# Performance work log

Hardware: AMD Instinct MI355X
Metric: run time of the kernel (lower is better)

## Reference

```python
import jax, jax.numpy as jnp
import numpy as np

# dims
N = 10000      # nodes
E = 320000     # edges (avg degree 32)
NS = 64        # hidden 0e scalar channels
NV = 64        # hidden 1o vector channels
EMB = 32       # node-attr embedding dim
NTYPES = 20    # max_atom_types
NB = 8         # number_of_basis (bessel)
RH = 16        # radial_neurons
L = 2          # layers
CUT = 3.5      # max_radius
NNEIGH = 32.0  # num_neighbors normalization
H = 0.1        # residual step size


def smooth_cutoff(u):
    # e3nn example smooth_cutoff applied to x/max_radius
    v = 2.0 * (u - 1.0)
    y = 0.5 * (1.0 - jnp.cos(jnp.pi * v))
    y = jnp.where(v > 0.0, 0.0, y)
    y = jnp.where(v < -1.0, 1.0, y)
    return y


def setup_inputs() -> dict:
    key = jax.random.key(0)
    ks = jax.random.split(key, 10)
    x = jax.random.normal(ks[0], (N, 6), jnp.float32)
    batch = jnp.zeros((N,), jnp.int32)
    node_attr = jax.random.randint(ks[1], (N,), 0, NTYPES)
    edge_src = jax.random.randint(ks[2], (E,), 0, N)
    # avoid self-loops (zero edge length -> NaN in sh / bessel)
    off = jax.random.randint(ks[3], (E,), 1, N)
    edge_dst = (edge_src + off) % N
    embed_table = 0.1 * jax.random.normal(ks[4], (NTYPES, EMB), jnp.float32)
    Ku = jax.random.normal(ks[5], (2, NV), jnp.float32)          # uplift (made semi-unitary via QR)
    W_sc_s = 0.05 * jax.random.normal(ks[6], (L, NS, EMB, NS + NV), jnp.float32)  # self-connection TP: scalars
    W_sc_v = 0.05 * jax.random.normal(ks[7], (L, NV, EMB, NV), jnp.float32)       # self-connection TP: vectors
    Wr1 = 0.3 * jax.random.normal(ks[8], (L, NB, RH), jnp.float32)
    br1 = jnp.zeros((L, RH), jnp.float32)
    Wr2 = 0.3 * jax.random.normal(ks[9], (L, RH, 4 * NV), jnp.float32)
    br2 = jnp.zeros((L, 4 * NV), jnp.float32)
    return {"x": x, "batch": batch, "node_attr": node_attr, "edge_src": edge_src,
            "edge_dst": edge_dst, "embed_table": embed_table, "Ku": Ku,
            "W_sc_s": W_sc_s, "W_sc_v": W_sc_v, "Wr1": Wr1, "br1": br1,
            "Wr2": Wr2, "br2": br2}


def reference(x, batch, node_attr, edge_src, edge_dst, embed_table, Ku,
              W_sc_s, W_sc_v, Wr1, br1, Wr2, br2):
    n = x.shape[0]
    a = embed_table[node_attr]                     # [n, EMB] node-attr embedding (0e scalars)
    # make uplift semi-unitary: Q^T Q = I_2
    Q, _ = jnp.linalg.qr(Ku.T)                     # [NV, 2]
    U = Q.T                                        # uplift [2, NV]
    x_v = x.reshape(n, 2, 3)                       # 2x1o: position, velocity
    y_s = jnp.zeros((n, NS), x.dtype)              # uplift has no 1o->0e path
    y_v = jnp.einsum('ncd,ch->nhd', x_v, U)        # [n, NV, 3]
    nfreq = jnp.arange(1, NB + 1, dtype=x.dtype)
    inv_deg = 1.0 / np.sqrt(NNEIGH)
    for l in range(L):
        pos = x_v[:, 0, :]
        ev = pos[edge_src] - pos[edge_dst]                          # [E, 3]
        elen = jnp.linalg.norm(ev, axis=1)                          # [E]
        sh = jnp.sqrt(3.0) * ev / elen[:, None]                     # 1x1o SH, component norm
        # bessel radial basis, scaled by sqrt(NB)
        bess = (jnp.sqrt(2.0 / CUT) * jnp.sin(jnp.pi * nfreq * elen[:, None] / CUT)
                / elen[:, None]) * np.sqrt(NB)                      # [E, NB]
        ea = smooth_cutoff(elen / CUT)[:, None] * sh                # edge_attr [E, 3]
        # radial MLP -> per-edge tensor-product weights (4 paths x NV channels)
        w = jax.nn.silu(bess @ Wr1[l] + br1[l]) @ Wr2[l] + br2[l]   # [E, 4*NV]
        wA, wB, wC, wD = jnp.split(w, 4, axis=1)
        s_src = y_s[edge_src]                                       # [E, NS]
        v_src = y_v[edge_src]                                       # [E, NV, 3]
        # TP paths: 0e x 1o -> 1o ; 1o x 1o -> 1o (cross) ; 1o x 1o -> 0e (dot, feats + gates)
        msg_v = (wA[:, :, None] * s_src[:, :, None] * ea[:, None, :]
                 + wC[:, :, None] * jnp.cross(v_src, ea[:, None, :]))  # [E, NV, 3]
        dots = jnp.einsum('evd,ed->ev', v_src, ea)                  # [E, NV]
        msg_s = jnp.concatenate([wB * dots, wD * dots], axis=1)     # [E, NS+NV]
        agg_s = jax.ops.segment_sum(msg_s, edge_dst, num_segments=n) * inv_deg
        agg_v = (jax.ops.segment_sum(msg_v.reshape(msg_v.shape[0], -1), edge_dst,
                                     num_segments=n).reshape(n, NV, 3) * inv_deg)
        # self-connection: fully-connected TP with node-attr scalars
        sc_s = jnp.einsum('ns,ne,seo->no', y_s, a, W_sc_s[l])       # [n, NS+NV]
        sc_v = jnp.einsum('nvd,ne,veu->nud', y_v, a, W_sc_v[l])     # [n, NV, 3]
        out_s = sc_s + agg_s
        out_v = sc_v + agg_v
        # gate: silu on scalar feats, sigmoid gates scale the vectors
        y_s = y_s + H * jax.nn.silu(out_s[:, :NS])
        y_v = y_v + H * jax.nn.sigmoid(out_s[:, NS:])[:, :, None] * out_v
        # project back to 2x1o
        x_v = jnp.einsum('nhd,hc->ncd', y_v, Q)
    return x_v.reshape(n, 6)
```

## Files before the change

### kernel.cpp

```cpp
#include <hip/hip_runtime.h>
#include <math.h>

#define NSC 64
#define NVC 64
#define EMB 32
#define NTYPES 20
#define NB 8
#define RH 16
#define LAYERS 2
#define CUTV 3.5f
#define HSTEP 0.1f

__global__ void qr_kernel(const float* __restrict__ Ku, float* __restrict__ Q)
{
  if (threadIdx.x != 0 || blockIdx.x != 0) return;
  float A0[64], A1[64], v0[64], v1[64], t1[64];
  for (int i = 0; i < 64; ++i) { A0[i] = Ku[i]; A1[i] = Ku[64 + i]; }
  float alpha = A0[0];
  float xn2 = 0.f;
  for (int i = 1; i < 64; ++i) xn2 += A0[i] * A0[i];
  float beta0 = -copysignf(sqrtf(alpha * alpha + xn2), alpha);
  float tau0 = (beta0 - alpha) / beta0;
  float inv0 = 1.f / (alpha - beta0);
  v0[0] = 1.f;
  for (int i = 1; i < 64; ++i) v0[i] = A0[i] * inv0;
  float w = 0.f;
  for (int i = 0; i < 64; ++i) w += v0[i] * A1[i];
  for (int i = 0; i < 64; ++i) A1[i] -= tau0 * w * v0[i];
  float alpha1 = A1[1];
  float xn2b = 0.f;
  for (int i = 2; i < 64; ++i) xn2b += A1[i] * A1[i];
  float beta1 = -copysignf(sqrtf(alpha1 * alpha1 + xn2b), alpha1);
  float tau1 = (beta1 - alpha1) / beta1;
  float inv1 = 1.f / (alpha1 - beta1);
  v1[0] = 0.f; v1[1] = 1.f;
  for (int i = 2; i < 64; ++i) v1[i] = A1[i] * inv1;
  for (int i = 0; i < 64; ++i) t1[i] = ((i == 1) ? 1.f : 0.f) - tau1 * v1[i];
  float d = 0.f;
  for (int i = 0; i < 64; ++i) d += v0[i] * t1[i];
  for (int i = 0; i < 64; ++i) {
    float q0 = ((i == 0) ? 1.f : 0.f) - tau0 * v0[i];
    float q1 = t1[i] - tau0 * d * v0[i];
    Q[i * 2 + 0] = q0;
    Q[i * 2 + 1] = q1;
  }
}

__global__ void init_state(const float* __restrict__ x, const float* __restrict__ Qm,
                           float* __restrict__ st0, int* __restrict__ cnt, int n)
{
  const int i = blockIdx.x * 256 + threadIdx.x;
  const int node = i >> 6, lane = i & 63;
  if (node < n) {
    const float q0 = Qm[lane * 2 + 0], q1 = Qm[lane * 2 + 1];
    const float* xp = x + (size_t)node * 6;
    float* sp = st0 + (size_t)node * 256 + lane;
    sp[0]   = 0.f;
    sp[64]  = xp[0] * q0 + xp[3] * q1;
    sp[128] = xp[1] * q0 + xp[4] * q1;
    sp[192] = xp[2] * q0 + xp[5] * q1;
  }
  if (i < n) cnt[i] = 0;
}

__global__ void hist_kernel(const int* __restrict__ edst, int* __restrict__ cnt, int m)
{
  const int e = blockIdx.x * 256 + threadIdx.x;
  if (e < m) atomicAdd(&cnt[edst[e]], 1);
}

__global__ void scan_kernel(int* cnt, int* off, int n)
{
  __shared__ int lds[1024];
  const int t = threadIdx.x;
  const int CH = (n + 1023) >> 10;
  const int base = t * CH;
  int local[16];
  int run = 0;
  for (int j = 0; j < CH; ++j) {
    int v = (base + j < n) ? cnt[base + j] : 0;
    local[j] = run;
    run += v;
  }
  lds[t] = run;
  __syncthreads();
  for (int s = 1; s < 1024; s <<= 1) {
    int v = (t >= s) ? lds[t - s] : 0;
    __syncthreads();
    lds[t] += v;
    __syncthreads();
  }
  const int excl = lds[t] - run;
  for (int j = 0; j < CH; ++j) {
    if (base + j < n) {
      int o = excl + local[j];
      off[base + j] = o;
      cnt[base + j] = o;
    }
  }
  if (t == 1023) off[n] = lds[1023];
}

__global__ void scatter_kernel(const int* __restrict__ edst, int* __restrict__ cursor,
                               int* __restrict__ csr, int m)
{
  const int e = blockIdx.x * 256 + threadIdx.x;
  if (e < m) {
    int p = atomicAdd(&cursor[edst[e]], 1);
    csr[p] = e;
  }
}

__global__ void reorder_kernel(const int* __restrict__ csr,
                               const int* __restrict__ esrc, const int* __restrict__ edst,
                               int* __restrict__ esrc_s, int* __restrict__ edst_s, int m)
{
  const int k = blockIdx.x * 256 + threadIdx.x;
  if (k < m) {
    const int e = csr[k];
    esrc_s[k] = esrc[e];
    edst_s[k] = edst[e];
  }
}

__global__ void type_weights(const float* __restrict__ embed,
                             const float* __restrict__ Wss,
                             const float* __restrict__ Wsv,
                             float* __restrict__ Ws, float* __restrict__ Wv,
                             int total_s, int total_v)
{
  const int i = blockIdx.x * 256 + threadIdx.x;
  if (i < total_s) {
    const int bid = i >> 13;
    const int p = i & 8191;
    const int l = bid / NTYPES, t = bid % NTYPES;
    const int s = p >> 7, o = p & 127;
    const float* ar = embed + t * EMB;
    const float* wp = Wss + ((size_t)(l * 64 + s) * EMB) * 128 + o;
    float acc = 0.f;
    #pragma unroll
    for (int e = 0; e < EMB; ++e) acc = fmaf(ar[e], wp[e * 128], acc);
    Ws[i] = acc;
  } else {
    const int j = i - total_s;
    if (j < total_v) {
      const int bid = j >> 12;
      const int p = j & 4095;
      const int l = bid / NTYPES, t = bid % NTYPES;
      const int v = p >> 6, u = p & 63;
      const float* ar = embed + t * EMB;
      const float* wp = Wsv + ((size_t)(l * 64 + v) * EMB) * 64 + u;
      float acc = 0.f;
      #pragma unroll
      for (int e = 0; e < EMB; ++e) acc = fmaf(ar[e], wp[e * 64], acc);
      Wv[j] = acc;
    }
  }
}

__global__ void edge_geom(const float* __restrict__ xv,
                          const int* __restrict__ esrc_s, const int* __restrict__ edst_s,
                          const float* __restrict__ Wr1l, const float* __restrict__ br1l,
                          float* __restrict__ egeo, int m)
{
  const int k = blockIdx.x * 256 + threadIdx.x;
  if (k >= m) return;
  const int s = esrc_s[k], d = edst_s[k];
  const float ex = xv[(size_t)s * 6 + 0] - xv[(size_t)d * 6 + 0];
  const float ey = xv[(size_t)s * 6 + 1] - xv[(size_t)d * 6 + 1];
  const float ez = xv[(size_t)s * 6 + 2] - xv[(size_t)d * 6 + 2];
  const float len = sqrtf(ex * ex + ey * ey + ez * ez);
  const float invl = 1.f / len;
  const float u = len * (1.f / CUTV);
  const float vv = 2.f * (u - 1.f);
  float cut = 0.5f * (1.f - cosf((float)M_PI * vv));
  cut = (vv > 0.f) ? 0.f : cut;
  cut = (vv < -1.f) ? 1.f : cut;
  const float cc = cut * 1.7320508075688772f * invl;
  float4* outp = (float4*)(egeo + (size_t)k * 20);
  outp[0] = make_float4(cc * ex, cc * ey, cc * ez, 0.f);
  float bess[NB];
  const float amp = 2.1380899352993948f * invl;
  const float arg = (float)M_PI * len * (1.f / CUTV);
  #pragma unroll
  for (int kk = 0; kk < NB; ++kk) bess[kk] = amp * sinf(arg * (float)(kk + 1));
  float hid[RH];
  #pragma unroll
  for (int j = 0; j < RH; ++j) {
    float h = br1l[j];
    #pragma unroll
    for (int kk = 0; kk < NB; ++kk) h = fmaf(bess[kk], Wr1l[kk * RH + j], h);
    hid[j] = h / (1.f + expf(-h));
  }
  outp[1] = make_float4(hid[0], hid[1], hid[2], hid[3]);
  outp[2] = make_float4(hid[4], hid[5], hid[6], hid[7]);
  outp[3] = make_float4(hid[8], hid[9], hid[10], hid[11]);
  outp[4] = make_float4(hid[12], hid[13], hid[14], hid[15]);
}

#define MLP_STEP(h, idx)                                                     \
  wA = fmaf((h), wr2A[idx], wA);                                             \
  wB = fmaf((h), wr2B[idx], wB);                                             \
  wC = fmaf((h), wr2C[idx], wC);                                             \
  wD = fmaf((h), wr2D[idx], wD);

__global__ __launch_bounds__(256, 2) void gather_update(
    const int* __restrict__ off, const int* __restrict__ esrc_s,
    const float* __restrict__ egeo,
    const float* __restrict__ st_in, const int* __restrict__ nattr,
    const float* __restrict__ Ws, const float* __restrict__ Wv,
    const float* __restrict__ Wr2l, const float* __restrict__ br2l,
    const float* __restrict__ Qm,
    float* __restrict__ st_out, float* __restrict__ xv_out, int n)
{
  const int lane = threadIdx.x & 63;
  const int node = blockIdx.x * 4 + (threadIdx.x >> 6);
  if (node >= n) return;

  float wr2A[RH], wr2B[RH], wr2C[RH], wr2D[RH];
  #pragma unroll
  for (int j = 0; j < RH; ++j) {
    const float* r = Wr2l + j * 256 + lane;
    wr2A[j] = r[0]; wr2B[j] = r[64]; wr2C[j] = r[128]; wr2D[j] = r[192];
  }
  const float bA = br2l[lane], bB = br2l[64 + lane],
              bC = br2l[128 + lane], bD = br2l[192 + lane];

  float aS1 = 0.f, aS2 = 0.f, aV0 = 0.f, aV1 = 0.f, aV2 = 0.f;
  const int k0 = off[node], k1 = off[node + 1];
  if (k0 < k1) {
    int srcN = esrc_s[k0];
    const float4* gN = (const float4*)(egeo + (size_t)k0 * 20);
    float4 N0 = gN[0], N1 = gN[1], N2 = gN[2], N3 = gN[3], N4 = gN[4];
    for (int k = k0; k < k1; ++k) {
      const int srcC = srcN;
      const float4 C0 = N0, C1 = N1, C2 = N2, C3 = N3, C4 = N4;
      const int kn = (k + 1 < k1) ? (k + 1) : k;
      srcN = esrc_s[kn];
      const float4* gp = (const float4*)(egeo + (size_t)kn * 20);
      N0 = gp[0]; N1 = gp[1]; N2 = gp[2]; N3 = gp[3]; N4 = gp[4];
      const float* pC = st_in + (size_t)srcC * 256 + lane;
      const float ss = pC[0], vx = pC[64], vy = pC[128], vz = pC[192];
      float wA = bA, wB = bB, wC = bC, wD = bD;
      MLP_STEP(C1.x, 0)  MLP_STEP(C1.y, 1)  MLP_STEP(C1.z, 2)  MLP_STEP(C1.w, 3)
      MLP_STEP(C2.x, 4)  MLP_STEP(C2.y, 5)  MLP_STEP(C2.z, 6)  MLP_STEP(C2.w, 7)
      MLP_STEP(C3.x, 8)  MLP_STEP(C3.y, 9)  MLP_STEP(C3.z, 10) MLP_STEP(C3.w, 11)
      MLP_STEP(C4.x, 12) MLP_STEP(C4.y, 13) MLP_STEP(C4.z, 14) MLP_STEP(C4.w, 15)
      const float dt = vx * C0.x + vy * C0.y + vz * C0.z;
      aS1 = fmaf(wB, dt, aS1);
      aS2 = fmaf(wD, dt, aS2);
      const float t = wA * ss;
      aV0 += t * C0.x + wC * (vy * C0.z - vz * C0.y);
      aV1 += t * C0.y + wC * (vz * C0.x - vx * C0.z);
      aV2 += t * C0.z + wC * (vx * C0.y - vy * C0.x);
    }
  }
  const float inv_deg = 0.17677669529663687f;

  const int ty = nattr[node];
  const float* WsT = Ws + (size_t)ty * 8192;
  const float* WvT = Wv + (size_t)ty * 4096;
  const float* own = st_in + (size_t)node * 256 + lane;
  const float ys_own = own[0], v0x = own[64], v0y = own[128], v0z = own[192];
  float oS1 = 0.f, oS2 = 0.f, oV0 = 0.f, oV1 = 0.f, oV2 = 0.f;
  #pragma unroll 4
  for (int s2 = 0; s2 < 64; ++s2) {
    const float yss = __shfl(ys_own, s2, 64);
    const float b0 = __shfl(v0x, s2, 64);
    const float b1 = __shfl(v0y, s2, 64);
    const float b2 = __shfl(v0z, s2, 64);
    const float wsA = WsT[s2 * 128 + lane];
    const float wsB = WsT[s2 * 128 + 64 + lane];
    const float wvv = WvT[s2 * 64 + lane];
    oS1 = fmaf(yss, wsA, oS1);
    oS2 = fmaf(yss, wsB, oS2);
    oV0 = fmaf(b0, wvv, oV0);
    oV1 = fmaf(b1, wvv, oV1);
    oV2 = fmaf(b2, wvv, oV2);
  }
  const float outS1 = oS1 + aS1 * inv_deg;
  const float outS2 = oS2 + aS2 * inv_deg;
  const float sig1 = 1.f / (1.f + expf(-outS1));
  const float gate = 1.f / (1.f + expf(-outS2));
  const float ysn = ys_own + HSTEP * outS1 * sig1;
  const float gf = HSTEP * gate;
  const float yvn0 = v0x + gf * (oV0 + aV0 * inv_deg);
  const float yvn1 = v0y + gf * (oV1 + aV1 * inv_deg);
  const float yvn2 = v0z + gf * (oV2 + aV2 * inv_deg);
  float* op = st_out + (size_t)node * 256 + lane;
  op[0] = ysn; op[64] = yvn0; op[128] = yvn1; op[192] = yvn2;

  const float q0 = Qm[lane * 2 + 0], q1 = Qm[lane * 2 + 1];
  float pr[6] = { yvn0 * q0, yvn1 * q0, yvn2 * q0,
                  yvn0 * q1, yvn1 * q1, yvn2 * q1 };
  #pragma unroll
  for (int mm = 1; mm < 64; mm <<= 1) {
    #pragma unroll
    for (int i = 0; i < 6; ++i) pr[i] += __shfl_xor(pr[i], mm, 64);
  }
  if (lane == 0) {
    #pragma unroll
    for (int i = 0; i < 6; ++i) xv_out[(size_t)node * 6 + i] = pr[i];
  }
}

extern "C" void kernel_launch(void* const* d_in, const int* in_sizes, int n_in,
                              void* d_out, int out_size, void* d_ws, size_t ws_size,
                              hipStream_t stream)
{
  const float* x     = (const float*)d_in[0];
  const int*   nattr = (const int*)d_in[2];
  const int*   esrc  = (const int*)d_in[3];
  const int*   edst  = (const int*)d_in[4];
  const float* embed = (const float*)d_in[5];
  const float* Ku    = (const float*)d_in[6];
  const float* Wss   = (const float*)d_in[7];
  const float* Wsv   = (const float*)d_in[8];
  const float* Wr1   = (const float*)d_in[9];
  const float* br1   = (const float*)d_in[10];
  const float* Wr2   = (const float*)d_in[11];
  const float* br2   = (const float*)d_in[12];
  const int n = in_sizes[0] / 6;
  const int m = in_sizes[3];

  char* p = (char*)d_ws;
  auto alloc = [&](size_t bytes) -> char* {
    char* r = p;
    p += (bytes + 255) & ~(size_t)255;
    return r;
  };
  int*   off    = (int*)alloc((size_t)(n + 1) * 4);
  int*   cursor = (int*)alloc((size_t)n * 4);
  int*   csr    = (int*)alloc((size_t)m * 4);
  int*   esrc_s = (int*)alloc((size_t)m * 4);
  int*   edst_s = (int*)alloc((size_t)m * 4);
  float* Q      = (float*)alloc(128 * 4);
  float* Ws     = (float*)alloc((size_t)LAYERS * NTYPES * 64 * 128 * 4);
  float* Wv     = (float*)alloc((size_t)LAYERS * NTYPES * 64 * 64 * 4);
  float* st0    = (float*)alloc((size_t)n * 256 * 4);
  float* st1    = (float*)alloc((size_t)n * 256 * 4);
  float* xvb    = (float*)alloc((size_t)n * 6 * 4);
  float* egeo   = (float*)alloc((size_t)m * 20 * 4);

  const int total_s = LAYERS * NTYPES * 64 * 128;
  const int total_v = LAYERS * NTYPES * 64 * 64;

  qr_kernel<<<1, 64, 0, stream>>>(Ku, Q);
  init_state<<<(n * 64 + 255) / 256, 256, 0, stream>>>(x, Q, st0, cursor, n);
  hist_kernel<<<(m + 255) / 256, 256, 0, stream>>>(edst, cursor, m);
  scan_kernel<<<1, 1024, 0, stream>>>(cursor, off, n);
  scatter_kernel<<<(m + 255) / 256, 256, 0, stream>>>(edst, cursor, csr, m);
  reorder_kernel<<<(m + 255) / 256, 256, 0, stream>>>(csr, esrc, edst, esrc_s, edst_s, m);
  type_weights<<<(total_s + total_v + 255) / 256, 256, 0, stream>>>(
      embed, Wss, Wsv, Ws, Wv, total_s, total_v);

  const float* xv_cur = x;
  const float* st_cur = st0;
  float* st_nxt = st1;
  for (int l = 0; l < LAYERS; ++l) {
    edge_geom<<<(m + 255) / 256, 256, 0, stream>>>(
        xv_cur, esrc_s, edst_s, Wr1 + l * NB * RH, br1 + l * RH, egeo, m);
    float* xv_out = (l == LAYERS - 1) ? (float*)d_out : xvb;
    gather_update<<<(n + 3) / 4, 256, 0, stream>>>(
        off, esrc_s, egeo, st_cur, nattr,
        Ws + (size_t)l * NTYPES * 8192, Wv + (size_t)l * NTYPES * 4096,
        Wr2 + l * RH * 256, br2 + l * 256, Q,
        st_nxt, xv_out, n);
    xv_cur = xv_out;
    float* ts = (float*)st_cur; st_cur = st_nxt; st_nxt = ts;
  }
}
```

Measured before the change: 343.5 us.

## Parallelize QR across a wave, use Chebyshev sines, prefetch source state, raise occupancy

The single-thread QR is replaced by a 64-lane version that uses wave shuffle reductions. Edge geometry now computes one sincos and derives the cutoff and all Bessel sines through the Chebyshev recurrence, instead of calling cosf plus eight sinf. The gather loop prefetches the next edge's source node state one iteration ahead and the next source index two ahead, hiding gather latency. Launch bounds rise to 3 blocks per CU, with an asm barrier to keep the MLP weights in VGPRs, which risks register spills.

```diff
diff --git a/kernel.cpp b/kernel.cpp
--- a/kernel.cpp
+++ b/kernel.cpp
@@ -11,39 +11,35 @@
 #define CUTV 3.5f
 #define HSTEP 0.1f
 
+__device__ __forceinline__ float wave_sum(float t)
+{
+  #pragma unroll
+  for (int mm = 1; mm < 64; mm <<= 1) t += __shfl_xor(t, mm, 64);
+  return t;
+}
+
 __global__ void qr_kernel(const float* __restrict__ Ku, float* __restrict__ Q)
 {
-  if (threadIdx.x != 0 || blockIdx.x != 0) return;
-  float A0[64], A1[64], v0[64], v1[64], t1[64];
-  for (int i = 0; i < 64; ++i) { A0[i] = Ku[i]; A1[i] = Ku[64 + i]; }
-  float alpha = A0[0];
-  float xn2 = 0.f;
-  for (int i = 1; i < 64; ++i) xn2 += A0[i] * A0[i];
-  float beta0 = -copysignf(sqrtf(alpha * alpha + xn2), alpha);
-  float tau0 = (beta0 - alpha) / beta0;
-  float inv0 = 1.f / (alpha - beta0);
-  v0[0] = 1.f;
-  for (int i = 1; i < 64; ++i) v0[i] = A0[i] * inv0;
-  float w = 0.f;
-  for (int i = 0; i < 64; ++i) w += v0[i] * A1[i];
-  for (int i = 0; i < 64; ++i) A1[i] -= tau0 * w * v0[i];
-  float alpha1 = A1[1];
-  float xn2b = 0.f;
-  for (int i = 2; i < 64; ++i) xn2b += A1[i] * A1[i];
-  float beta1 = -copysignf(sqrtf(alpha1 * alpha1 + xn2b), alpha1);
-  float tau1 = (beta1 - alpha1) / beta1;
-  float inv1 = 1.f / (alpha1 - beta1);
-  v1[0] = 0.f; v1[1] = 1.f;
-  for (int i = 2; i < 64; ++i) v1[i] = A1[i] * inv1;
-  for (int i = 0; i < 64; ++i) t1[i] = ((i == 1) ? 1.f : 0.f) - tau1 * v1[i];
-  float d = 0.f;
-  for (int i = 0; i < 64; ++i) d += v0[i] * t1[i];
-  for (int i = 0; i < 64; ++i) {
-    float q0 = ((i == 0) ? 1.f : 0.f) - tau0 * v0[i];
-    float q1 = t1[i] - tau0 * d * v0[i];
-    Q[i * 2 + 0] = q0;
-    Q[i * 2 + 1] = q1;
-  }
+  const int i = threadIdx.x;
+  float a0 = Ku[i], a1 = Ku[64 + i];
+  const float xn2 = wave_sum((i >= 1) ? a0 * a0 : 0.f);
+  const float alpha = __shfl(a0, 0, 64);
+  const float beta0 = -copysignf(sqrtf(alpha * alpha + xn2), alpha);
+  const float tau0 = (beta0 - alpha) / beta0;
+  const float inv0 = 1.f / (alpha - beta0);
+  const float v0 = (i == 0) ? 1.f : a0 * inv0;
+  const float w = wave_sum(v0 * a1);
+  a1 -= tau0 * w * v0;
+  const float alpha1 = __shfl(a1, 1, 64);
+  const float xn2b = wave_sum((i >= 2) ? a1 * a1 : 0.f);
+  const float beta1 = -copysignf(sqrtf(alpha1 * alpha1 + xn2b), alpha1);
+  const float tau1 = (beta1 - alpha1) / beta1;
+  const float inv1 = 1.f / (alpha1 - beta1);
+  const float v1 = (i == 0) ? 0.f : ((i == 1) ? 1.f : a1 * inv1);
+  const float t1v = ((i == 1) ? 1.f : 0.f) - tau1 * v1;
+  const float d = wave_sum(v0 * t1v);
+  Q[i * 2 + 0] = ((i == 0) ? 1.f : 0.f) - tau0 * v0;
+  Q[i * 2 + 1] = t1v - tau0 * d * v0;
 }
 
 __global__ void init_state(const float* __restrict__ x, const float* __restrict__ Qm,
@@ -172,8 +168,11 @@
   const float len = sqrtf(ex * ex + ey * ey + ez * ez);
   const float invl = 1.f / len;
   const float u = len * (1.f / CUTV);
+  const float arg = (float)M_PI * u;
+  float sa, ca;
+  __sincosf(arg, &sa, &ca);
   const float vv = 2.f * (u - 1.f);
-  float cut = 0.5f * (1.f - cosf((float)M_PI * vv));
+  float cut = 0.5f * (1.f - (2.f * ca * ca - 1.f));
   cut = (vv > 0.f) ? 0.f : cut;
   cut = (vv < -1.f) ? 1.f : cut;
   const float cc = cut * 1.7320508075688772f * invl;
@@ -181,9 +180,14 @@
   outp[0] = make_float4(cc * ex, cc * ey, cc * ez, 0.f);
   float bess[NB];
   const float amp = 2.1380899352993948f * invl;
-  const float arg = (float)M_PI * len * (1.f / CUTV);
-  #pragma unroll
-  for (int kk = 0; kk < NB; ++kk) bess[kk] = amp * sinf(arg * (float)(kk + 1));
+  const float twoc = 2.f * ca;
+  float sm1 = 0.f, scur = sa;
+  #pragma unroll
+  for (int kk = 0; kk < NB; ++kk) {
+    bess[kk] = amp * scur;
+    const float snext = twoc * scur - sm1;
+    sm1 = scur; scur = snext;
+  }
   float hid[RH];
   #pragma unroll
   for (int j = 0; j < RH; ++j) {
@@ -204,7 +208,7 @@
   wC = fmaf((h), wr2C[idx], wC);                                             \
   wD = fmaf((h), wr2D[idx], wD);
 
-__global__ __launch_bounds__(256, 2) void gather_update(
+__global__ __launch_bounds__(256, 3) void gather_update(
     const int* __restrict__ off, const int* __restrict__ esrc_s,
     const float* __restrict__ egeo,
     const float* __restrict__ st_in, const int* __restrict__ nattr,
@@ -223,24 +227,31 @@
     const float* r = Wr2l + j * 256 + lane;
     wr2A[j] = r[0]; wr2B[j] = r[64]; wr2C[j] = r[128]; wr2D[j] = r[192];
   }
+  #pragma unroll
+  for (int j = 0; j < RH; ++j) {
+    asm volatile("" : "+v"(wr2A[j]), "+v"(wr2B[j]), "+v"(wr2C[j]), "+v"(wr2D[j]));
+  }
   const float bA = br2l[lane], bB = br2l[64 + lane],
               bC = br2l[128 + lane], bD = br2l[192 + lane];
 
   float aS1 = 0.f, aS2 = 0.f, aV0 = 0.f, aV1 = 0.f, aV2 = 0.f;
   const int k0 = off[node], k1 = off[node + 1];
   if (k0 < k1) {
-    int srcN = esrc_s[k0];
-    const float4* gN = (const float4*)(egeo + (size_t)k0 * 20);
-    float4 N0 = gN[0], N1 = gN[1], N2 = gN[2], N3 = gN[3], N4 = gN[4];
+    const int src0 = esrc_s[k0];
+    const float* p0 = st_in + (size_t)src0 * 256 + lane;
+    float ssN = p0[0], vxN = p0[64], vyN = p0[128], vzN = p0[192];
+    const float4* g0 = (const float4*)(egeo + (size_t)k0 * 20);
+    float4 N0 = g0[0], N1 = g0[1], N2 = g0[2], N3 = g0[3], N4 = g0[4];
+    int srcN = (k0 + 1 < k1) ? esrc_s[k0 + 1] : src0;
     for (int k = k0; k < k1; ++k) {
-      const int srcC = srcN;
+      const float ss = ssN, vx = vxN, vy = vyN, vz = vzN;
       const float4 C0 = N0, C1 = N1, C2 = N2, C3 = N3, C4 = N4;
+      const float* pN = st_in + (size_t)srcN * 256 + lane;
+      ssN = pN[0]; vxN = pN[64]; vyN = pN[128]; vzN = pN[192];
       const int kn = (k + 1 < k1) ? (k + 1) : k;
-      srcN = esrc_s[kn];
       const float4* gp = (const float4*)(egeo + (size_t)kn * 20);
       N0 = gp[0]; N1 = gp[1]; N2 = gp[2]; N3 = gp[3]; N4 = gp[4];
-      const float* pC = st_in + (size_t)srcC * 256 + lane;
-      const float ss = pC[0], vx = pC[64], vy = pC[128], vz = pC[192];
+      srcN = (k + 2 < k1) ? esrc_s[k + 2] : srcN;
       float wA = bA, wB = bB, wC = bC, wD = bD;
       MLP_STEP(C1.x, 0)  MLP_STEP(C1.y, 1)  MLP_STEP(C1.z, 2)  MLP_STEP(C1.w, 3)
       MLP_STEP(C2.x, 4)  MLP_STEP(C2.y, 5)  MLP_STEP(C2.z, 6)  MLP_STEP(C2.w, 7)
```

After: 317.9 us. 1.08x faster.
